# Kernel optimization log

Hardware: AMD Instinct MI355X
Metric: run time of the kernel (lower is better)

Reference implementation:

```python
import jax, jax.numpy as jnp
import numpy as np
import math

B, L, E, H, K = 4, 1024, 1024, 16, 64
D = E // H  # head_dim = 64; rel_pe has 2K+1 = 129 rows


def setup_inputs() -> dict:
    key = jax.random.key(0)
    ks = jax.random.split(key, 4)
    s = 1.0 / math.sqrt(E)
    return {
        "q": jax.random.normal(ks[0], (B, L, E), dtype=jnp.float32),
        "in_proj_weight": jax.random.normal(ks[1], (3 * E, E), dtype=jnp.float32) * s,
        "in_proj_bias": jnp.zeros((3 * E,), dtype=jnp.float32),
        "out_w": jax.random.normal(ks[2], (E, E), dtype=jnp.float32) * s,
        "out_b": jnp.zeros((E,), dtype=jnp.float32),
        "rel_pe": jax.random.normal(ks[3], (2 * K + 1, D), dtype=jnp.float32) * (1.0 / math.sqrt(D)),
    }


def _attend(q, in_proj_weight, in_proj_bias, out_w, out_b, rel_pe):
    b, l, e = q.shape
    h, d = H, D
    qkv = q @ in_proj_weight.T + in_proj_bias  # (B, L, 3E)
    qh, kh, vh = jnp.split(qkv, 3, axis=-1)
    # (B, L, E) -> (B, H, L, D)
    qh = qh.reshape(b, l, h, d).transpose(0, 2, 1, 3)
    kh = kh.reshape(b, l, h, d).transpose(0, 2, 1, 3)
    vh = vh.reshape(b, l, h, d).transpose(0, 2, 1, 3)
    qh = qh / math.sqrt(d)  # scaling applies to both content and position terms
    # content scores
    scores = jnp.einsum("bhid,bhjd->bhij", qh, kh)
    # relative-position bias: a[i, j] = rel_pe[clip(j - i, -K, K) + K]
    # compute q . rel_pe once, then gather per (i, j) -- same math as the
    # original O(L^2 * D) materialized tensor, without building it.
    pos = jnp.arange(l)
    rel = jnp.clip(pos[None, :] - pos[:, None], -K, K) + K  # (L, L) int
    bias_r = jnp.einsum("bhid,rd->bhir", qh, rel_pe)  # (B, H, L, 2K+1)
    bias = jnp.take_along_axis(bias_r, jnp.broadcast_to(rel[None, None], (b, h, l, l)), axis=-1)
    attn = jax.nn.softmax(scores + bias, axis=-1)
    out = jnp.einsum("bhij,bhjd->bhid", attn, vh)  # (B, H, L, D)
    out = out.transpose(0, 2, 1, 3).reshape(b, l, e)
    return out @ out_w.T + out_b


def reference(q, in_proj_weight, in_proj_bias, out_w, out_b, rel_pe):
    return _attend(q, in_proj_weight, in_proj_bias, out_w, out_b, rel_pe)
```

## Files before the change

kernel.cpp:

```cpp
#include <hip/hip_runtime.h>
#include <math.h>

typedef _Float16 half_t;
typedef _Float16 half8 __attribute__((ext_vector_type(8)));
typedef _Float16 half4v __attribute__((ext_vector_type(4)));
typedef float float4v __attribute__((ext_vector_type(4)));

#define AS1 __attribute__((address_space(1)))
#define AS3 __attribute__((address_space(3)))

#define MFMA16(a, b, c) __builtin_amdgcn_mfma_f32_16x16x32_f16((a), (b), (c), 0, 0, 0)

__device__ __forceinline__ void gload16(const half_t* g, half_t* l) {
    __builtin_amdgcn_global_load_lds((const AS1 void*)g, (AS3 void*)l, 16, 0, 0);
}

__device__ __forceinline__ int iclamp(int v, int lo, int hi) {
    return v < lo ? lo : (v > hi ? hi : v);
}

__global__ __launch_bounds__(256) void cast_kernel(
    const float* __restrict__ q, const float* __restrict__ w_in,
    const float* __restrict__ w_out, const float* __restrict__ pe,
    half_t* __restrict__ q16, half_t* __restrict__ w16,
    half_t* __restrict__ wo16, half_t* __restrict__ pe16)
{
    const int tid = blockIdx.x * 256 + threadIdx.x;
    const int stride = gridDim.x * 256;
    for (int i = tid; i < 1048576; i += stride) {
        float4 v = ((const float4*)q)[i];
        *(half4v*)(q16 + (size_t)i * 4) =
            (half4v){(half_t)v.x, (half_t)v.y, (half_t)v.z, (half_t)v.w};
    }
    for (int i = tid; i < 786432; i += stride) {
        float4 v = ((const float4*)w_in)[i];
        *(half4v*)(w16 + (size_t)i * 4) =
            (half4v){(half_t)v.x, (half_t)v.y, (half_t)v.z, (half_t)v.w};
    }
    for (int i = tid; i < 262144; i += stride) {
        float4 v = ((const float4*)w_out)[i];
        *(half4v*)(wo16 + (size_t)i * 4) =
            (half4v){(half_t)v.x, (half_t)v.y, (half_t)v.z, (half_t)v.w};
    }
    for (int i = tid; i < 2064; i += stride) {
        float4 v = ((const float4*)pe)[i];
        *(half4v*)(pe16 + (size_t)i * 4) =
            (half4v){(half_t)v.x, (half_t)v.y, (half_t)v.z, (half_t)v.w};
    }
    for (int i = tid; i < 240; i += stride) {
        *(half4v*)(pe16 + 8256 + (size_t)i * 4) = (half4v){0, 0, 0, 0};
    }
}

__global__ __launch_bounds__(256) void qkv_gemm(
    const half_t* __restrict__ A, const half_t* __restrict__ W,
    const float* __restrict__ bias,
    half_t* __restrict__ qh, half_t* __restrict__ kh, half_t* __restrict__ vt)
{
    __shared__ half_t As[128 * 32];
    __shared__ half_t Bs[128 * 32];
    const int K = 1024;
    const int tid = threadIdx.x, lane = tid & 63, wid = tid >> 6;
    const int wm = wid & 1, wn = wid >> 1;
    const int bid = blockIdx.x;
    const int xcd = bid & 7, idx = bid >> 3;
    const int m0 = (((xcd >> 1) << 3) + (idx & 7)) * 128;
    const int n0 = (((xcd & 1) * 12) + (idx >> 3)) * 128;

    const half_t* gA[2]; const half_t* gB[2];
    half_t* lA[2]; half_t* lB[2];
    {
        const int base = wid * 128;
#pragma unroll
        for (int c = 0; c < 2; ++c) {
            int slot = base + c * 64 + lane;
            int row = slot >> 2;
            int ch = (slot & 3) ^ ((row >> 1) & 3);
            gA[c] = A + (size_t)(m0 + row) * K + ch * 8;
            gB[c] = W + (size_t)(n0 + row) * K + ch * 8;
            lA[c] = As + (base + c * 64) * 8;
            lB[c] = Bs + (base + c * 64) * 8;
        }
    }
    int aOff[4], bOff[4];
#pragma unroll
    for (int i = 0; i < 4; ++i) {
        int ra = wm * 64 + i * 16 + (lane & 15);
        aOff[i] = ra * 32 + (((lane >> 4) ^ ((ra >> 1) & 3)) * 8);
        int rb = wn * 64 + i * 16 + (lane & 15);
        bOff[i] = rb * 32 + (((lane >> 4) ^ ((rb >> 1) & 3)) * 8);
    }
    float4v acc[4][4];
#pragma unroll
    for (int i = 0; i < 4; ++i)
#pragma unroll
        for (int j = 0; j < 4; ++j) acc[i][j] = (float4v){0.f, 0.f, 0.f, 0.f};

    for (int k0 = 0; k0 < K; k0 += 32) {
        __syncthreads();
        gload16(gA[0], lA[0]); gload16(gA[1], lA[1]);
        gload16(gB[0], lB[0]); gload16(gB[1], lB[1]);
        gA[0] += 32; gA[1] += 32; gB[0] += 32; gB[1] += 32;
        __syncthreads();
        half8 af[4], bf[4];
#pragma unroll
        for (int i = 0; i < 4; ++i) af[i] = *(const half8*)(As + aOff[i]);
#pragma unroll
        for (int j = 0; j < 4; ++j) bf[j] = *(const half8*)(Bs + bOff[j]);
#pragma unroll
        for (int i = 0; i < 4; ++i)
#pragma unroll
            for (int j = 0; j < 4; ++j)
                acc[i][j] = MFMA16(af[i], bf[j], acc[i][j]);
    }

    const int part = n0 >> 10;
#pragma unroll
    for (int ni = 0; ni < 4; ++ni) {
        const int col = n0 + wn * 64 + ni * 16 + (lane & 15);
        const float bv = bias[col];
        const int hh = (col >> 6) & 15, d = col & 63;
#pragma unroll
        for (int mi = 0; mi < 4; ++mi) {
            const int r0 = m0 + wm * 64 + mi * 16 + ((lane >> 4) << 2);
            const int bb = r0 >> 10, l0 = r0 & 1023;
            if (part == 0) {
#pragma unroll
                for (int r = 0; r < 4; ++r)
                    qh[(((size_t)(bb * 16 + hh) * 1024) + l0 + r) * 64 + d] =
                        (half_t)((acc[mi][ni][r] + bv) * 0.125f);
            } else if (part == 1) {
#pragma unroll
                for (int r = 0; r < 4; ++r)
                    kh[(((size_t)(bb * 16 + hh) * 1024) + l0 + r) * 64 + d] =
                        (half_t)(acc[mi][ni][r] + bv);
            } else {
                half4v pk;
#pragma unroll
                for (int r = 0; r < 4; ++r) pk[r] = (half_t)(acc[mi][ni][r] + bv);
                *(half4v*)(vt + ((size_t)(bb * 16 + hh) * 64 + d) * 1024 + l0) = pk;
            }
        }
    }
}

__global__ __launch_bounds__(256) void out_gemm(
    const half_t* __restrict__ A, const half_t* __restrict__ W,
    const float* __restrict__ bias, float* __restrict__ C)
{
    __shared__ half_t As[128 * 32];
    __shared__ half_t Bs[64 * 32];
    const int K = 1024;
    const int tid = threadIdx.x, lane = tid & 63, wid = tid >> 6;
    const int wm = wid & 1, wn = wid >> 1;
    const int bid = blockIdx.x;
    const int xcd = bid & 7, idx = bid >> 3;
    const int m0 = ((xcd << 2) + (idx >> 4)) * 128;
    const int n0 = (idx & 15) * 64;

    const half_t* gA[2]; const half_t* gB1;
    half_t* lA[2]; half_t* lB1;
    {
        const int base = wid * 128;
#pragma unroll
        for (int c = 0; c < 2; ++c) {
            int slot = base + c * 64 + lane;
            int row = slot >> 2;
            int ch = (slot & 3) ^ ((row >> 1) & 3);
            gA[c] = A + (size_t)(m0 + row) * K + ch * 8;
            lA[c] = As + (base + c * 64) * 8;
        }
        int slotB = wid * 64 + lane;
        int rowB = slotB >> 2;
        int chB = (slotB & 3) ^ ((rowB >> 1) & 3);
        gB1 = W + (size_t)(n0 + rowB) * K + chB * 8;
        lB1 = Bs + (wid * 64) * 8;
    }
    int aOff[4], bOff[2];
#pragma unroll
    for (int i = 0; i < 4; ++i) {
        int ra = wm * 64 + i * 16 + (lane & 15);
        aOff[i] = ra * 32 + (((lane >> 4) ^ ((ra >> 1) & 3)) * 8);
    }
#pragma unroll
    for (int j = 0; j < 2; ++j) {
        int rb = wn * 32 + j * 16 + (lane & 15);
        bOff[j] = rb * 32 + (((lane >> 4) ^ ((rb >> 1) & 3)) * 8);
    }
    float4v acc[4][2];
#pragma unroll
    for (int i = 0; i < 4; ++i)
#pragma unroll
        for (int j = 0; j < 2; ++j) acc[i][j] = (float4v){0.f, 0.f, 0.f, 0.f};

    for (int k0 = 0; k0 < K; k0 += 32) {
        __syncthreads();
        gload16(gA[0], lA[0]); gload16(gA[1], lA[1]);
        gload16(gB1, lB1);
        gA[0] += 32; gA[1] += 32; gB1 += 32;
        __syncthreads();
        half8 af[4], bf[2];
#pragma unroll
        for (int i = 0; i < 4; ++i) af[i] = *(const half8*)(As + aOff[i]);
#pragma unroll
        for (int j = 0; j < 2; ++j) bf[j] = *(const half8*)(Bs + bOff[j]);
#pragma unroll
        for (int i = 0; i < 4; ++i)
#pragma unroll
            for (int j = 0; j < 2; ++j)
                acc[i][j] = MFMA16(af[i], bf[j], acc[i][j]);
    }

#pragma unroll
    for (int ni = 0; ni < 2; ++ni) {
        const int col = n0 + wn * 32 + ni * 16 + (lane & 15);
        const float bv = bias[col];
#pragma unroll
        for (int mi = 0; mi < 4; ++mi) {
            const int r0 = m0 + wm * 64 + mi * 16 + ((lane >> 4) << 2);
#pragma unroll
            for (int r = 0; r < 4; ++r)
                C[(size_t)(r0 + r) * 1024 + col] = acc[mi][ni][r] + bv;
        }
    }
}

__global__ __launch_bounds__(256) void attn_mfma(
    const half_t* __restrict__ qh, const half_t* __restrict__ kh,
    const half_t* __restrict__ vt, const half_t* __restrict__ pe,
    half_t* __restrict__ ao)
{
    __shared__ half_t KV[8192];
    __shared__ half_t Pm[4 * 1024];
    __shared__ half_t R2[4 * 16 * 156];

    const int tid = threadIdx.x, lane = tid & 63, wid = tid >> 6;
    const int bid = blockIdx.x;
    const int xcd = bid & 7, idx = bid >> 3;
    const int bh = xcd + ((idx >> 4) << 3);
    const int q0 = (idx & 15) * 64;
    const int h = bh & 15, b = bh >> 4;
    const int i0 = q0 + wid * 16;
    const size_t hbase = (size_t)(b * 16 + h) * 64 * 1024;
    const half_t* Qg = qh + hbase;
    const half_t* Kg = kh + hbase;
    const half_t* Vg = vt + hbase;

    const int qrow = i0 + (lane & 15);
    const half8 qa0 = *(const half8*)(Qg + (size_t)qrow * 64 + ((lane >> 4) << 3));
    const half8 qa1 = *(const half8*)(Qg + (size_t)qrow * 64 + 32 + ((lane >> 4) << 3));

    const half_t* gS[4]; int lOff[4]; int ginc[4];
#pragma unroll
    for (int c = 0; c < 4; ++c) {
        const int slot0 = wid * 256 + c * 64;
        const int slot = slot0 + lane;
        if (slot0 < 512) {
            int srow = slot >> 3, sch = (slot & 7) ^ (srow & 7);
            gS[c] = Kg + srow * 64 + sch * 8;
            ginc[c] = 64 * 64;
            lOff[c] = slot0 * 8;
        } else {
            int s2 = slot - 512;
            int srow = s2 >> 3, sch = (s2 & 7) ^ (srow & 7);
            gS[c] = Vg + srow * 1024 + sch * 8;
            ginc[c] = 64;
            lOff[c] = 4096 + (slot0 - 512) * 8;
        }
    }

    half_t* r2w = R2 + wid * (16 * 156);
#pragma unroll
    for (int rj = 0; rj < 9; ++rj) {
        const int prow = rj * 16 + (lane & 15);
        half8 pb0 = *(const half8*)(pe + prow * 64 + ((lane >> 4) << 3));
        half8 pb1 = *(const half8*)(pe + prow * 64 + 32 + ((lane >> 4) << 3));
        float4v c = (float4v){0.f, 0.f, 0.f, 0.f};
        c = MFMA16(qa0, pb0, c);
        c = MFMA16(qa1, pb1, c);
        const int col = rj * 16 + (lane & 15);
        if (col < 129) {
#pragma unroll
            for (int r = 0; r < 4; ++r) {
                const int il = ((lane >> 4) << 2) + r;
                const half_t hv = (half_t)(c[r] - 2.0f);
                if (col == 0) {
                    for (int ts = 0; ts <= il + 4; ++ts) r2w[il * 156 + ts] = hv;
                } else if (col == 128) {
                    for (int ts = il + 132; ts < 152; ++ts) r2w[il * 156 + ts] = hv;
                } else {
                    r2w[il * 156 + col + 4 + il] = hv;
                }
            }
        }
    }

    int kOff[4][2], vOff[4][2], pOff[2];
#pragma unroll
    for (int nj = 0; nj < 4; ++nj)
#pragma unroll
        for (int kc = 0; kc < 2; ++kc) {
            int row = nj * 16 + (lane & 15);
            int ch = (kc * 4 + (lane >> 4)) ^ (row & 7);
            kOff[nj][kc] = row * 64 + ch * 8;
            vOff[nj][kc] = 4096 + row * 64 + ch * 8;
        }
    {
        const int m = lane & 15;
#pragma unroll
        for (int kc = 0; kc < 2; ++kc)
            pOff[kc] = wid * 1024 + m * 64 + ((kc * 32 + ((lane >> 4) << 3)) ^ ((m & 7) * 8));
    }
    const int pwBase = wid * 1024 + (lane & 15) * 64;
    const int pwSw = ((lane & 15) & 7) * 8;

    float l4[4] = {0.f, 0.f, 0.f, 0.f};
    float4v oacc[4];
#pragma unroll
    for (int ni = 0; ni < 4; ++ni) oacc[ni] = (float4v){0.f, 0.f, 0.f, 0.f};

    for (int kt = 0; kt < 16; ++kt) {
        __syncthreads();
#pragma unroll
        for (int c = 0; c < 4; ++c) { gload16(gS[c], KV + lOff[c]); gS[c] += ginc[c]; }
        __syncthreads();

        const int kv0 = kt * 64;
        const half_t* r2row = r2w + (lane & 15) * 156;
        float4v s[4];
#pragma unroll
        for (int nj = 0; nj < 4; ++nj) {
            int traw = kv0 + nj * 16 + ((lane >> 4) << 2) + 64 - i0;
            int tsb = iclamp(traw, -4, 144) + 4;
            half4v bh4 = *(const half4v*)(r2row + tsb);
            float4v t;
#pragma unroll
            for (int r = 0; r < 4; ++r) t[r] = (float)bh4[r];
            half8 k0 = *(const half8*)(KV + kOff[nj][0]);
            half8 k1 = *(const half8*)(KV + kOff[nj][1]);
            t = MFMA16(k0, qa0, t);
            t = MFMA16(k1, qa1, t);
            s[nj] = t;
        }

#pragma unroll
        for (int nj = 0; nj < 4; ++nj) {
            half4v ph;
#pragma unroll
            for (int r = 0; r < 4; ++r) {
                float p = __expf(s[nj][r]);
                l4[r] += p;
                ph[r] = (half_t)p;
            }
            const int kvb = nj * 16 + ((lane >> 4) << 2);
            *(half4v*)(Pm + pwBase + (kvb ^ pwSw)) = ph;
        }

        half8 pf0 = *(const half8*)(Pm + pOff[0]);
        half8 pf1 = *(const half8*)(Pm + pOff[1]);
#pragma unroll
        for (int ni = 0; ni < 4; ++ni) {
            half8 v0 = *(const half8*)(KV + vOff[ni][0]);
            half8 v1 = *(const half8*)(KV + vOff[ni][1]);
            oacc[ni] = MFMA16(v0, pf0, oacc[ni]);
            oacc[ni] = MFMA16(v1, pf1, oacc[ni]);
        }
    }

    float l_r = (l4[0] + l4[1]) + (l4[2] + l4[3]);
    l_r += __shfl_xor(l_r, 16);
    l_r += __shfl_xor(l_r, 32);

    const float inv = 1.0f / l_r;
    const int row_g = i0 + (lane & 15);
    half_t* aorow = ao + ((size_t)(b * 1024 + row_g)) * 1024 + h * 64;
#pragma unroll
    for (int ni = 0; ni < 4; ++ni) {
        const int d0 = ni * 16 + ((lane >> 4) << 2);
        half4v oh;
#pragma unroll
        for (int r = 0; r < 4; ++r) oh[r] = (half_t)(oacc[ni][r] * inv);
        *(half4v*)(aorow + d0) = oh;
    }
}

extern "C" void kernel_launch(void* const* d_in, const int* in_sizes, int n_in,
                              void* d_out, int out_size, void* d_ws, size_t ws_size,
                              hipStream_t stream) {
    const float* q     = (const float*)d_in[0];
    const float* w_in  = (const float*)d_in[1];
    const float* b_in  = (const float*)d_in[2];
    const float* w_out = (const float*)d_in[3];
    const float* b_out = (const float*)d_in[4];
    const float* pe    = (const float*)d_in[5];
    float* out = (float*)d_out;

    half_t* ws = (half_t*)d_ws;
    half_t* q16   = ws;
    half_t* w16   = q16 + 4194304;
    half_t* wo16  = w16 + 3145728;
    half_t* pe16  = wo16 + 1048576;
    half_t* qh16  = pe16 + 9216;
    half_t* kh16  = qh16 + 4194304;
    half_t* vt16  = kh16 + 4194304;
    half_t* ao16  = vt16 + 4194304;

    cast_kernel<<<2048, 256, 0, stream>>>(q, w_in, w_out, pe, q16, w16, wo16, pe16);
    qkv_gemm<<<768, 256, 0, stream>>>(q16, w16, b_in, qh16, kh16, vt16);
    attn_mfma<<<1024, 256, 0, stream>>>(qh16, kh16, vt16, pe16, ao16);
    out_gemm<<<512, 256, 0, stream>>>(ao16, wo16, b_out, out);
}
```

Baseline: 188.3 us.

## Switch attention kernel to 32x32 MFMA tiles with 128-query blocks

Rewrites the attention kernel to use 32x32x16 MFMA instructions. Each wave now handles 32 query rows instead of 16 and each block 128 queries, so the grid is halved to 512 blocks. Every K/V tile loaded into LDS is reused across twice as many queries, which cuts global and LDS traffic per output and the number of MFMA issues. The cost is more registers and LDS per block (bigger P and relative-bias buffers), fewer blocks for latency hiding, and a larger zero-padded rel_pe buffer with shifted workspace offsets.

```diff
diff --git a/kernel.cpp b/kernel.cpp
--- a/kernel.cpp
+++ b/kernel.cpp
@@ -5,11 +5,13 @@
 typedef _Float16 half8 __attribute__((ext_vector_type(8)));
 typedef _Float16 half4v __attribute__((ext_vector_type(4)));
 typedef float float4v __attribute__((ext_vector_type(4)));
+typedef float float16v __attribute__((ext_vector_type(16)));
 
 #define AS1 __attribute__((address_space(1)))
 #define AS3 __attribute__((address_space(3)))
 
 #define MFMA16(a, b, c) __builtin_amdgcn_mfma_f32_16x16x32_f16((a), (b), (c), 0, 0, 0)
+#define MFMA32(a, b, c) __builtin_amdgcn_mfma_f32_32x32x16_f16((a), (b), (c), 0, 0, 0)
 
 __device__ __forceinline__ void gload16(const half_t* g, half_t* l) {
     __builtin_amdgcn_global_load_lds((const AS1 void*)g, (AS3 void*)l, 16, 0, 0);
@@ -47,7 +49,7 @@
         *(half4v*)(pe16 + (size_t)i * 4) =
             (half4v){(half_t)v.x, (half_t)v.y, (half_t)v.z, (half_t)v.w};
     }
-    for (int i = tid; i < 240; i += stride) {
+    for (int i = tid; i < 496; i += stride) {
         *(half4v*)(pe16 + 8256 + (size_t)i * 4) = (half4v){0, 0, 0, 0};
     }
 }
@@ -231,24 +233,27 @@
     half_t* __restrict__ ao)
 {
     __shared__ half_t KV[8192];
-    __shared__ half_t Pm[4 * 1024];
-    __shared__ half_t R2[4 * 16 * 156];
+    __shared__ half_t Pm[4 * 2048];
+    __shared__ half_t R2[4 * 32 * 172];
 
     const int tid = threadIdx.x, lane = tid & 63, wid = tid >> 6;
+    const int hl = lane >> 5, ql = lane & 31;
     const int bid = blockIdx.x;
     const int xcd = bid & 7, idx = bid >> 3;
-    const int bh = xcd + ((idx >> 4) << 3);
-    const int q0 = (idx & 15) * 64;
+    const int bh = xcd + ((idx >> 3) << 3);
+    const int q0 = (idx & 7) * 128;
     const int h = bh & 15, b = bh >> 4;
-    const int i0 = q0 + wid * 16;
+    const int i0w = q0 + wid * 32;
     const size_t hbase = (size_t)(b * 16 + h) * 64 * 1024;
     const half_t* Qg = qh + hbase;
     const half_t* Kg = kh + hbase;
     const half_t* Vg = vt + hbase;
 
-    const int qrow = i0 + (lane & 15);
-    const half8 qa0 = *(const half8*)(Qg + (size_t)qrow * 64 + ((lane >> 4) << 3));
-    const half8 qa1 = *(const half8*)(Qg + (size_t)qrow * 64 + 32 + ((lane >> 4) << 3));
+    const int qrow = i0w + ql;
+    half8 qb[4];
+#pragma unroll
+    for (int cc = 0; cc < 4; ++cc)
+        qb[cc] = *(const half8*)(Qg + (size_t)qrow * 64 + cc * 16 + hl * 8);
 
     const half_t* gS[4]; int lOff[4]; int ginc[4];
 #pragma unroll
@@ -269,55 +274,59 @@
         }
     }
 
-    half_t* r2w = R2 + wid * (16 * 156);
-#pragma unroll
-    for (int rj = 0; rj < 9; ++rj) {
-        const int prow = rj * 16 + (lane & 15);
-        half8 pb0 = *(const half8*)(pe + prow * 64 + ((lane >> 4) << 3));
-        half8 pb1 = *(const half8*)(pe + prow * 64 + 32 + ((lane >> 4) << 3));
-        float4v c = (float4v){0.f, 0.f, 0.f, 0.f};
-        c = MFMA16(qa0, pb0, c);
-        c = MFMA16(qa1, pb1, c);
-        const int col = rj * 16 + (lane & 15);
+    half_t* r2w = R2 + wid * (32 * 172);
+#pragma unroll
+    for (int j2 = 0; j2 < 5; ++j2) {
+        float16v c;
+#pragma unroll
+        for (int r = 0; r < 16; ++r) c[r] = 0.f;
+#pragma unroll
+        for (int cc = 0; cc < 4; ++cc) {
+            half8 pb = *(const half8*)(pe + (size_t)(j2 * 32 + ql) * 64 + cc * 16 + hl * 8);
+            c = MFMA32(qb[cc], pb, c);
+        }
+        const int col = j2 * 32 + ql;
         if (col < 129) {
 #pragma unroll
-            for (int r = 0; r < 4; ++r) {
-                const int il = ((lane >> 4) << 2) + r;
-                const half_t hv = (half_t)(c[r] - 2.0f);
+            for (int reg = 0; reg < 16; ++reg) {
+                const int il = (reg & 3) + 8 * (reg >> 2) + 4 * hl;
+                const half_t hv = (half_t)(c[reg] - 2.0f);
                 if (col == 0) {
-                    for (int ts = 0; ts <= il + 4; ++ts) r2w[il * 156 + ts] = hv;
+                    for (int ts = 0; ts <= il + 4; ++ts) r2w[il * 172 + ts] = hv;
                 } else if (col == 128) {
-                    for (int ts = il + 132; ts < 152; ++ts) r2w[il * 156 + ts] = hv;
+                    for (int ts = il + 132; ts <= il + 139; ++ts) r2w[il * 172 + ts] = hv;
                 } else {
-                    r2w[il * 156 + col + 4 + il] = hv;
+                    r2w[il * 172 + col + 4 + il] = hv;
                 }
             }
         }
     }
 
-    int kOff[4][2], vOff[4][2], pOff[2];
-#pragma unroll
-    for (int nj = 0; nj < 4; ++nj)
-#pragma unroll
-        for (int kc = 0; kc < 2; ++kc) {
-            int row = nj * 16 + (lane & 15);
-            int ch = (kc * 4 + (lane >> 4)) ^ (row & 7);
-            kOff[nj][kc] = row * 64 + ch * 8;
-            vOff[nj][kc] = 4096 + row * 64 + ch * 8;
-        }
-    {
-        const int m = lane & 15;
-#pragma unroll
-        for (int kc = 0; kc < 2; ++kc)
-            pOff[kc] = wid * 1024 + m * 64 + ((kc * 32 + ((lane >> 4) << 3)) ^ ((m & 7) * 8));
-    }
-    const int pwBase = wid * 1024 + (lane & 15) * 64;
-    const int pwSw = ((lane & 15) & 7) * 8;
-
-    float l4[4] = {0.f, 0.f, 0.f, 0.f};
-    float4v oacc[4];
-#pragma unroll
-    for (int ni = 0; ni < 4; ++ni) oacc[ni] = (float4v){0.f, 0.f, 0.f, 0.f};
+    int kOff[2][4], vOff[2][4], pOff[4];
+#pragma unroll
+    for (int t2 = 0; t2 < 2; ++t2)
+#pragma unroll
+        for (int cc = 0; cc < 4; ++cc) {
+            int row = t2 * 32 + ql;
+            int ch = (cc * 2 + hl) ^ (row & 7);
+            kOff[t2][cc] = row * 64 + ch * 8;
+            vOff[t2][cc] = 4096 + row * 64 + ch * 8;
+        }
+    const int pwSw = (ql & 7) * 8;
+    const int pwBase = wid * 2048 + ql * 64;
+#pragma unroll
+    for (int cc = 0; cc < 4; ++cc)
+        pOff[cc] = pwBase + ((cc * 16 + hl * 8) ^ pwSw);
+
+    const int hiC = 128 + ((ql + 3) & ~3);
+    const half_t* r2row = r2w + ql * 172;
+
+    float l_r = 0.f;
+    float16v oacc[2];
+#pragma unroll
+    for (int dt = 0; dt < 2; ++dt)
+#pragma unroll
+        for (int r = 0; r < 16; ++r) oacc[dt][r] = 0.f;
 
     for (int kt = 0; kt < 16; ++kt) {
         __syncthreads();
@@ -325,63 +334,62 @@
         for (int c = 0; c < 4; ++c) { gload16(gS[c], KV + lOff[c]); gS[c] += ginc[c]; }
         __syncthreads();
 
-        const int kv0 = kt * 64;
-        const half_t* r2row = r2w + (lane & 15) * 156;
-        float4v s[4];
-#pragma unroll
-        for (int nj = 0; nj < 4; ++nj) {
-            int traw = kv0 + nj * 16 + ((lane >> 4) << 2) + 64 - i0;
-            int tsb = iclamp(traw, -4, 144) + 4;
-            half4v bh4 = *(const half4v*)(r2row + tsb);
-            float4v t;
-#pragma unroll
-            for (int r = 0; r < 4; ++r) t[r] = (float)bh4[r];
-            half8 k0 = *(const half8*)(KV + kOff[nj][0]);
-            half8 k1 = *(const half8*)(KV + kOff[nj][1]);
-            t = MFMA16(k0, qa0, t);
-            t = MFMA16(k1, qa1, t);
-            s[nj] = t;
-        }
-
-#pragma unroll
-        for (int nj = 0; nj < 4; ++nj) {
-            half4v ph;
-#pragma unroll
-            for (int r = 0; r < 4; ++r) {
-                float p = __expf(s[nj][r]);
-                l4[r] += p;
-                ph[r] = (half_t)p;
-            }
-            const int kvb = nj * 16 + ((lane >> 4) << 2);
-            *(half4v*)(Pm + pwBase + (kvb ^ pwSw)) = ph;
-        }
-
-        half8 pf0 = *(const half8*)(Pm + pOff[0]);
-        half8 pf1 = *(const half8*)(Pm + pOff[1]);
-#pragma unroll
-        for (int ni = 0; ni < 4; ++ni) {
-            half8 v0 = *(const half8*)(KV + vOff[ni][0]);
-            half8 v1 = *(const half8*)(KV + vOff[ni][1]);
-            oacc[ni] = MFMA16(v0, pf0, oacc[ni]);
-            oacc[ni] = MFMA16(v1, pf1, oacc[ni]);
-        }
-    }
-
-    float l_r = (l4[0] + l4[1]) + (l4[2] + l4[3]);
-    l_r += __shfl_xor(l_r, 16);
+#pragma unroll
+        for (int t2 = 0; t2 < 2; ++t2) {
+            float16v s;
+#pragma unroll
+            for (int g = 0; g < 4; ++g) {
+                int traw = kt * 64 + t2 * 32 + 8 * g + 4 * hl + 64 - i0w;
+                int tsb = iclamp(traw, -4, hiC) + 4;
+                half4v bh4 = *(const half4v*)(r2row + tsb);
+#pragma unroll
+                for (int r = 0; r < 4; ++r) s[4 * g + r] = (float)bh4[r];
+            }
+#pragma unroll
+            for (int cc = 0; cc < 4; ++cc) {
+                half8 kf = *(const half8*)(KV + kOff[t2][cc]);
+                s = MFMA32(kf, qb[cc], s);
+            }
+#pragma unroll
+            for (int g = 0; g < 4; ++g) {
+                half4v ph;
+#pragma unroll
+                for (int r = 0; r < 4; ++r) {
+                    float p = __expf(s[4 * g + r]);
+                    l_r += p;
+                    ph[r] = (half_t)p;
+                }
+                const int kvb = t2 * 32 + 8 * g + 4 * hl;
+                *(half4v*)(Pm + pwBase + (kvb ^ pwSw)) = ph;
+            }
+        }
+
+        half8 pf[4];
+#pragma unroll
+        for (int cc = 0; cc < 4; ++cc) pf[cc] = *(const half8*)(Pm + pOff[cc]);
+#pragma unroll
+        for (int dt = 0; dt < 2; ++dt)
+#pragma unroll
+            for (int cc = 0; cc < 4; ++cc) {
+                half8 vf = *(const half8*)(KV + vOff[dt][cc]);
+                oacc[dt] = MFMA32(vf, pf[cc], oacc[dt]);
+            }
+    }
+
     l_r += __shfl_xor(l_r, 32);
-
     const float inv = 1.0f / l_r;
-    const int row_g = i0 + (lane & 15);
-    half_t* aorow = ao + ((size_t)(b * 1024 + row_g)) * 1024 + h * 64;
-#pragma unroll
-    for (int ni = 0; ni < 4; ++ni) {
-        const int d0 = ni * 16 + ((lane >> 4) << 2);
-        half4v oh;
-#pragma unroll
-        for (int r = 0; r < 4; ++r) oh[r] = (half_t)(oacc[ni][r] * inv);
-        *(half4v*)(aorow + d0) = oh;
-    }
+
+    half_t* aorow = ao + ((size_t)(b * 1024 + i0w + ql)) * 1024 + h * 64;
+#pragma unroll
+    for (int dt = 0; dt < 2; ++dt)
+#pragma unroll
+        for (int g = 0; g < 4; ++g) {
+            const int d0 = dt * 32 + 8 * g + 4 * hl;
+            half4v oh;
+#pragma unroll
+            for (int r = 0; r < 4; ++r) oh[r] = (half_t)(oacc[dt][4 * g + r] * inv);
+            *(half4v*)(aorow + d0) = oh;
+        }
 }
 
 extern "C" void kernel_launch(void* const* d_in, const int* in_sizes, int n_in,
@@ -400,13 +408,13 @@
     half_t* w16   = q16 + 4194304;
     half_t* wo16  = w16 + 3145728;
     half_t* pe16  = wo16 + 1048576;
-    half_t* qh16  = pe16 + 9216;
+    half_t* qh16  = pe16 + 10240;
     half_t* kh16  = qh16 + 4194304;
     half_t* vt16  = kh16 + 4194304;
     half_t* ao16  = vt16 + 4194304;
 
     cast_kernel<<<2048, 256, 0, stream>>>(q, w_in, w_out, pe, q16, w16, wo16, pe16);
     qkv_gemm<<<768, 256, 0, stream>>>(q16, w16, b_in, qh16, kh16, vt16);
-    attn_mfma<<<1024, 256, 0, stream>>>(qh16, kh16, vt16, pe16, ao16);
+    attn_mfma<<<512, 256, 0, stream>>>(qh16, kh16, vt16, pe16, ao16);
     out_gemm<<<512, 256, 0, stream>>>(ao16, wo16, b_out, out);
 }
```

Measured after the change: 182.3 us. -3.2%, faster.
